# Optimization experiments

Measured on AMD Instinct MI355X. Metric: run time of the kernel, lower is better.

The kernel has to match this reference:

```python
import jax, jax.numpy as jnp
import numpy as np

PATCH = 64
STRIDE = PATCH // 2
SEQ = 65536
NPATCH = (SEQ - PATCH) // STRIDE + 1  # 2047
B = 256
EPS = 1e-5


def setup_inputs() -> dict:
    key = jax.random.key(0)
    ks = jax.random.split(key, 10)
    s = lambda k, shp: jax.random.normal(k, shp, jnp.float32) * 0.05
    return dict(
        x=jax.random.normal(ks[0], (B, 1, SEQ), jnp.float32),
        conv1_w=s(ks[1], (NPATCH, NPATCH - 1)),
        conv1_b=s(ks[2], (NPATCH,)),
        w1=s(ks[3], (32, 3, 5)), b1=s(ks[4], (32,)),
        g1=jnp.ones((32,), jnp.float32), be1=jnp.zeros((32,), jnp.float32),
        w2=s(ks[5], (64, 32, 3)), b2=s(ks[6], (64,)),
        g2=jnp.ones((64,), jnp.float32), be2=jnp.zeros((64,), jnp.float32),
        w3=s(ks[7], (128, 64, 3)), b3=s(ks[8], (128,)),
        g3=jnp.ones((128,), jnp.float32), be3=jnp.zeros((128,), jnp.float32),
    )


def _conv1d(x, w, b, pad):
    # x: [B, Cin, L], w: [Cout, Cin, K]
    y = jax.lax.conv_general_dilated(x, w, (1,), [(pad, pad)],
                                     dimension_numbers=('NCH', 'OIH', 'NCH'))
    return y + b[None, :, None]


def _bn(x, g, be):
    # training-mode BatchNorm1d: biased var over (batch, length)
    m = jnp.mean(x, axis=(0, 2), keepdims=True)
    v = jnp.var(x, axis=(0, 2), keepdims=True)
    return (x - m) * jax.lax.rsqrt(v + EPS) * g[None, :, None] + be[None, :, None]


def _maxpool2(x):
    # MaxPool1d(kernel=2, stride=2), floor division of length
    L = x.shape[-1] // 2
    return x[..., : 2 * L].reshape(x.shape[0], x.shape[1], L, 2).max(-1)


def reference(x, conv1_w, conv1_b, w1, b1, g1, be1, w2, b2, g2, be2, w3, b3, g3, be3):
    starts = jnp.arange(NPATCH) * STRIDE
    idx = starts[:, None] + jnp.arange(PATCH)[None, :]         # [NW, W]
    xp = x[:, :, idx]                                          # [B,1,NW,W]
    mean = xp.mean(-1)                                         # [B,1,NW]
    std = jnp.std(xp, axis=-1, ddof=1)                         # torch.std is unbiased
    stats = jnp.concatenate([mean, std], axis=1)               # [B,2,NW]
    dx = jnp.diff(xp, axis=2)                                  # diff across window index: [B,1,NW-1,W]
    dmax = dx.max(-1)                                          # [B,1,NW-1]
    dmax = jnp.transpose(dmax, (0, 2, 1))                      # [B,NW-1,1]
    # conv1: 1x1 Conv1d over length-1 axis == matmul over channel dim
    d2 = jnp.einsum('oi,bil->bol', conv1_w, dmax) + conv1_b[None, :, None]  # [B,NW,1]
    d2 = jnp.transpose(d2, (0, 2, 1))                          # [B,1,NW]
    x3 = jnp.concatenate([stats, d2], axis=1)                  # [B,3,NW]
    h = _maxpool2(jax.nn.relu(_bn(_conv1d(x3, w1, b1, 2), g1, be1)))
    h = _maxpool2(jax.nn.relu(_bn(_conv1d(h, w2, b2, 1), g2, be2)))
    h = jax.nn.relu(_bn(_conv1d(h, w3, b3, 1), g3, be3))
    return h.mean(-1)                                          # AdaptiveAvgPool1d(1)+Flatten -> [B,128]
```

## Files before the change

kernel.cpp:

```cpp
#include <hip/hip_runtime.h>
#include <math.h>

#define NB 256
#define SEQ 65536
#define NP 2047
#define NPM 2046
#define KPAD 2048
#define LEN1 2047
#define LEN2 1023
#define LEN3 511
#define C1 32
#define C2 64
#define C3 128
#define NPART 2048
#define NPART2 (NB*4)
#define LPAD 514
#define LPAD1 1026

#define OFF_X3   0
#define SZ_X3    (NB*3*NP)
#define OFF_DMAX (OFF_X3 + SZ_X3)
#define SZ_DMAX  (NB*NPM)
#define OFF_Y1   (OFF_DMAX + SZ_DMAX)
#define SZ_Y1    (NB*C1*LEN1)
#define OFF_Y2   (OFF_Y1 + SZ_Y1)
#define SZ_Y2    (NB*C2*LEN2)
#define OFF_S1   (OFF_Y2 + SZ_Y2)
#define OFF_S2   (OFF_S1 + 2*C1)
#define OFF_S3   (OFF_S2 + 2*C2)
#define OFF_W2C  (OFF_S3 + 2*C3)
#define OFF_W3B  (OFF_W2C + C1*C2*3)
#define OFF_PS   (OFF_W3B + C2*C3*3)
#define OFF_PQ   (OFF_PS + C3*NPART)
#define OFF_WB   OFF_Y2
#define OFF_H1R  OFF_Y2
#define OFF_H2T  OFF_Y2
#define OFF_H1B  OFF_Y1
#define OFF_PM   (OFF_Y1 + (NB*LPAD1*C1)/2)
#define OFF_W2B  OFF_W2C

typedef __attribute__((ext_vector_type(8))) short short8;
typedef __attribute__((ext_vector_type(4))) float f32x4;

__device__ inline short f2bf(float f){
  union { float f; unsigned u; } x; x.f = f;
  unsigned r = x.u + 0x7FFF + ((x.u >> 16) & 1);
  return (short)(r >> 16);
}

#define RED4L(v) v += __shfl_xor(v,1,64); v += __shfl_xor(v,2,64); \
                 v += __shfl_xor(v,4,64); v += __shfl_xor(v,8,64);

#define TILES(X) X(0,0) X(0,1) X(0,2) X(0,3) X(1,0) X(1,1) X(1,2) X(1,3) \
                 X(2,0) X(2,1) X(2,2) X(2,3) X(3,0) X(3,1) X(3,2) X(3,3)
#define DECLBIAS(P,ct) f32x4 bi##ct = *(const f32x4*)((P) + cbase + ct*16 + kq*4);
#define DECLACC(lt,ct) f32x4 acc##lt##ct = bi##ct;

__global__ __launch_bounds__(256) void k_patch(const float* __restrict__ x, const float* __restrict__ c1b,
                                               float* __restrict__ ws){
  float* x3    = ws + OFF_X3;
  short* dmaxB = (short*)(ws + OFF_DMAX);
  int b = blockIdx.y;
  int chunk = blockIdx.x;
  const float* xr = x + (size_t)b*SEQ + chunk*2048;
  __shared__ float Ss[65], Qs[65], Dm[65];
  int w = threadIdx.x >> 6;
  int l = threadIdx.x & 63;
  #pragma unroll
  for (int i=0;i<2;i++){
    int seg = w*2 + i;
    int off = seg*256;
    float4 A = *(const float4*)(xr + off + l*4);
    float4 Bh = make_float4(0.f,0.f,0.f,0.f);
    if (l >= 56){
      int g = chunk*2048 + off + 256 + (l-56)*4;
      if (g + 3 < SEQ) Bh = *(const float4*)(xr + off + 256 + (l-56)*4);
    }
    int src = (l+8) & 63;
    float p0 = __shfl(A.x, src, 64), p1 = __shfl(A.y, src, 64),
          p2 = __shfl(A.z, src, 64), p3 = __shfl(A.w, src, 64);
    if (l >= 56){ p0=Bh.x; p1=Bh.y; p2=Bh.z; p3=Bh.w; }
    float s = (A.x+A.y)+(A.z+A.w);
    float q = fmaf(A.x,A.x, fmaf(A.y,A.y, fmaf(A.z,A.z, A.w*A.w)));
    float d = fmaxf(fmaxf(p0-A.x, p1-A.y), fmaxf(p2-A.z, p3-A.w));
    #pragma unroll
    for (int o=1;o<8;o<<=1){
      s += __shfl_xor(s,o,64);
      q += __shfl_xor(q,o,64);
      d  = fmaxf(d, __shfl_xor(d,o,64));
    }
    if ((l&7)==0){ int m = seg*8 + (l>>3); Ss[m]=s; Qs[m]=q; Dm[m]=d; }
  }
  if (w==0){
    float s=0.f,q=0.f,d=-1e30f;
    if (l < 8){
      int g = chunk*2048 + 2048 + l*4;
      if (g+3 < SEQ){
        float4 A = *(const float4*)(xr + 2048 + l*4);
        float4 P = make_float4(0.f,0.f,0.f,0.f);
        if (g+35 < SEQ) P = *(const float4*)(xr + 2048 + 32 + l*4);
        s = (A.x+A.y)+(A.z+A.w);
        q = fmaf(A.x,A.x, fmaf(A.y,A.y, fmaf(A.z,A.z, A.w*A.w)));
        d = fmaxf(fmaxf(P.x-A.x, P.y-A.y), fmaxf(P.z-A.z, P.w-A.w));
      }
    }
    #pragma unroll
    for (int o=1;o<8;o<<=1){
      s += __shfl_xor(s,o,64);
      q += __shfl_xor(q,o,64);
      d  = fmaxf(d, __shfl_xor(d,o,64));
    }
    if (l==0){ Ss[64]=s; Qs[64]=q; Dm[64]=d; }
  }
  __syncthreads();
  if (threadIdx.x < 64){
    int j = threadIdx.x;
    int p = chunk*64 + j;
    if (p < NP){
      float S = Ss[j]+Ss[j+1];
      float Q = Qs[j]+Qs[j+1];
      float mean = S*(1.0f/64.0f);
      float var  = (Q - S*mean)*(1.0f/63.0f);
      x3[(b*3+0)*NP + p] = mean;
      x3[(b*3+1)*NP + p] = sqrtf(fmaxf(var,0.0f));
      x3[(b*3+2)*NP + p] = c1b[p];
    }
    dmaxB[(size_t)b*KPAD + p] = (p < NPM) ? f2bf(fmaxf(Dm[j], Dm[j+1])) : (short)0;
  }
}

__global__ __launch_bounds__(256) void k_wB(const float* __restrict__ W, float* __restrict__ ws){
  short* Wb = (short*)(ws + OFF_WB);
  int o = blockIdx.y;
  int k = blockIdx.x*256 + threadIdx.x;
  Wb[(size_t)o*KPAD + k] = (k < NPM) ? f2bf(W[(size_t)o*NPM + k]) : (short)0;
}

__global__ __launch_bounds__(256) void k_wt(const float* __restrict__ w2, const float* __restrict__ w3, float* __restrict__ ws){
  short* w2b = (short*)(ws + OFF_W2B);
  short* w3b = (short*)(ws + OFF_W3B);
  int t = blockIdx.x*256 + threadIdx.x;
  if (t < 3*C2*C1){
    int tap = t / (C2*C1);
    int r = t - tap*(C2*C1);
    int c = r >> 5, i = r & 31;
    w2b[t] = f2bf(w2[(c*C1 + i)*3 + tap]);
  }
  if (t < 3*C3*C2){
    int tap = t / (C3*C2);
    int r = t - tap*(C3*C2);
    int c = r / C2, i = r - c*C2;
    w3b[(tap*C3 + c)*C2 + i] = f2bf(w3[(c*C2+i)*3 + tap]);
  }
}

__global__ __launch_bounds__(256) void k_gemm(float* __restrict__ ws){
  const short* Ab = (const short*)(ws + OFF_DMAX);
  const short* Bb = (const short*)(ws + OFF_WB);
  float* x3 = ws + OFF_X3;
  int wid  = __builtin_amdgcn_readfirstlane(threadIdx.x >> 6);
  int lane = threadIdx.x & 63;
  int ln = lane & 15, kq = lane >> 4;
  int n0  = blockIdx.x*32;
  int m16 = (blockIdx.y*4 + wid)*16;
  int ks  = blockIdx.z*512;
  f32x4 acc0 = {0.f,0.f,0.f,0.f}, acc1 = {0.f,0.f,0.f,0.f};
  int o0 = n0 + ln, o1 = n0 + 16 + ln;
  const short* ap  = Ab + (size_t)(m16 + ln)*KPAD + ks + kq*8;
  const short* bp0 = Bb + (size_t)min(o0, NP-1)*KPAD + ks + kq*8;
  const short* bp1 = Bb + (size_t)min(o1, NP-1)*KPAD + ks + kq*8;
  #pragma unroll 4
  for (int s=0; s<16; s++){
    short8 av = *(const short8*)(ap  + s*32);
    short8 b0 = *(const short8*)(bp0 + s*32);
    short8 b1 = *(const short8*)(bp1 + s*32);
    acc0 = __builtin_amdgcn_mfma_f32_16x16x32_bf16(av, b0, acc0, 0, 0, 0);
    acc1 = __builtin_amdgcn_mfma_f32_16x16x32_bf16(av, b1, acc1, 0, 0, 0);
  }
  #pragma unroll
  for (int r=0;r<4;r++){
    int b = m16 + kq*4 + r;
    float* xp = x3 + ((size_t)b*3 + 2)*NP;
    if (o0 < NP) atomicAdd(xp + o0, acc0[r]);
    if (o1 < NP) atomicAdd(xp + o1, acc1[r]);
  }
}

__global__ __launch_bounds__(256) void k_conv1f(const float* __restrict__ w1, const float* __restrict__ b1, float* __restrict__ ws){
  const float* x3 = ws + OFF_X3;
  float* h1r = ws + OFF_H1R;
  float* ps = ws + OFF_PS;
  float* pq = ws + OFF_PQ;
  int b = blockIdx.y;
  int blk = blockIdx.x;
  int w = threadIdx.x >> 6;
  int lane = threadIdx.x & 63;
  int h = lane >> 5, c = lane & 31;
  int p0 = blk*256 + w*64 + h*32;
  float wv[3][5];
  #pragma unroll
  for (int i=0;i<3;i++){
    #pragma unroll
    for (int j=0;j<5;j++) wv[i][j] = w1[(c*3+i)*5+j];
  }
  float bc = b1[c];
  const float* xb = x3 + (size_t)b*3*NP;
  float s = 0.f, q = 0.f;
  #pragma unroll
  for (int k0=0;k0<32;k0+=8){
    float xv[3][12];
    #pragma unroll
    for (int i=0;i<3;i++){
      #pragma unroll
      for (int t=0;t<12;t++){
        int g = p0 + k0 - 2 + t;
        xv[i][t] = (g >= 0 && g < LEN1) ? xb[(size_t)i*NP + g] : 0.f;
      }
    }
    float acc[8];
    #pragma unroll
    for (int k=0;k<8;k++){
      float a = bc;
      #pragma unroll
      for (int i=0;i<3;i++){
        #pragma unroll
        for (int j=0;j<5;j++) a = fmaf(wv[i][j], xv[i][k+j], a);
      }
      acc[k] = a;
      if (p0 + k0 + k < LEN1){ s += a; q = fmaf(a, a, q); }
    }
    #pragma unroll
    for (int t=0;t<4;t++){
      int m = ((p0 + k0) >> 1) + t;
      if (m < LEN2) h1r[((size_t)b*LEN2 + m)*C1 + c] = fmaxf(acc[2*t], acc[2*t+1]);
    }
  }
  s += __shfl_xor(s, 32, 64);
  q += __shfl_xor(q, 32, 64);
  __shared__ float es[4][C1], eq[4][C1];
  if (h == 0){ es[w][c] = s; eq[w][c] = q; }
  __syncthreads();
  if (threadIdx.x < C1){
    int cc = threadIdx.x;
    float S = es[0][cc]+es[1][cc]+es[2][cc]+es[3][cc];
    float Q = eq[0][cc]+eq[1][cc]+eq[2][cc]+eq[3][cc];
    ps[(size_t)cc*NPART + b*8 + blk] = S;
    pq[(size_t)cc*NPART + b*8 + blk] = Q;
  }
}

__global__ __launch_bounds__(256) void k_fin(const float* __restrict__ ps, const float* __restrict__ pq,
                                             const float* __restrict__ g, const float* __restrict__ be,
                                             float* __restrict__ stats, int C, int npart, double invN,
                                             float* __restrict__ outz){
  if (outz) outz[(size_t)threadIdx.x * C3 + blockIdx.x] = 0.f;
  int c = blockIdx.x;
  double s=0.0, q=0.0;
  for (int j=threadIdx.x; j<npart; j+=256){ s += (double)ps[c*npart+j]; q += (double)pq[c*npart+j]; }
  #pragma unroll
  for (int off=32; off; off>>=1){ s += __shfl_xor(s,off,64); q += __shfl_xor(q,off,64); }
  __shared__ double rs[4], rq[4];
  int wid = threadIdx.x>>6, lane=threadIdx.x&63;
  if (lane==0){ rs[wid]=s; rq[wid]=q; }
  __syncthreads();
  if (threadIdx.x==0){
    double S = rs[0]+rs[1]+rs[2]+rs[3];
    double Q = rq[0]+rq[1]+rq[2]+rq[3];
    double mean = S*invN;
    double var  = Q*invN - mean*mean;
    double a = (double)g[c] / sqrt(var + 1e-5);
    stats[c]   = (float)a;
    stats[C+c] = (float)((double)be[c] - mean*a);
  }
}

__global__ __launch_bounds__(256) void k_bn1t(float* __restrict__ ws){
  const float* st = ws + OFF_S1;
  const float* h1r = ws + OFF_H1R;
  short* h1b = (short*)(ws + OFF_H1B);
  int b = blockIdx.y;
  int idx8 = (blockIdx.x*256 + threadIdx.x)*8;
  if (idx8 >= LPAD1*C1) return;
  int row = idx8 >> 5, i0 = idx8 & 31;
  short* dst = h1b + ((size_t)b*LPAD1 + row)*C1 + i0;
  short8 r;
  if (row == 0 || row >= 1024){
    r = (short8)0;
  } else {
    const float* src = h1r + ((size_t)b*LEN2 + (row-1))*C1 + i0;
    f32x4 vlo = *(const f32x4*)src, vhi = *(const f32x4*)(src+4);
    f32x4 alo = *(const f32x4*)(st + i0),      ahi = *(const f32x4*)(st + i0 + 4);
    f32x4 blo = *(const f32x4*)(st + C1 + i0), bhi = *(const f32x4*)(st + C1 + i0 + 4);
    #pragma unroll
    for (int j=0;j<4;j++){
      r[j]   = f2bf(fmaxf(fmaf(alo[j], vlo[j], blo[j]), 0.f));
      r[j+4] = f2bf(fmaxf(fmaf(ahi[j], vhi[j], bhi[j]), 0.f));
    }
  }
  *(short8*)dst = r;
}

__global__ __launch_bounds__(256) void k_conv2m(const float* __restrict__ b2, float* __restrict__ ws){
  const short* h1b = (const short*)(ws + OFF_H1B);
  const short* w2b = (const short*)(ws + OFF_W2B);
  float* pmaxT = ws + OFF_PM;
  float* ps = ws + OFF_PS;
  float* pq = ws + OFF_PQ;
  int b   = blockIdx.y;
  int blk = blockIdx.x;
  int w   = __builtin_amdgcn_readfirstlane(threadIdx.x >> 6);
  int lane = threadIdx.x & 63;
  int ln = lane & 15, kq = lane >> 4;
  int l0 = blk*256 + w*64;
  int cbase = 0;
  DECLBIAS(b2,0) DECLBIAS(b2,1) DECLBIAS(b2,2) DECLBIAS(b2,3)
  TILES(DECLACC)
  const short* wA = w2b + (size_t)ln*C1 + kq*8;
#define LDW(T,ct) short8 aw##T##ct = *(const short8*)(wA + (size_t)(T*C2 + ct*16)*C1);
  LDW(0,0) LDW(0,1) LDW(0,2) LDW(0,3)
  LDW(1,0) LDW(1,1) LDW(1,2) LDW(1,3)
  LDW(2,0) LDW(2,1) LDW(2,2) LDW(2,3)
#undef LDW
  const short* hB = h1b + ((size_t)b*LPAD1 + l0 + ln)*C1 + kq*8;
#define MMT0(lt,ct) acc##lt##ct = __builtin_amdgcn_mfma_f32_16x16x32_bf16(aw0##ct, bv##lt, acc##lt##ct, 0, 0, 0);
#define MMT1(lt,ct) acc##lt##ct = __builtin_amdgcn_mfma_f32_16x16x32_bf16(aw1##ct, bv##lt, acc##lt##ct, 0, 0, 0);
#define MMT2(lt,ct) acc##lt##ct = __builtin_amdgcn_mfma_f32_16x16x32_bf16(aw2##ct, bv##lt, acc##lt##ct, 0, 0, 0);
#define CSTEP(T) { \
    short8 bv0 = *(const short8*)(hB + (size_t)(0*16 + T)*C1); \
    short8 bv1 = *(const short8*)(hB + (size_t)(1*16 + T)*C1); \
    short8 bv2 = *(const short8*)(hB + (size_t)(2*16 + T)*C1); \
    short8 bv3 = *(const short8*)(hB + (size_t)(3*16 + T)*C1); \
    TILES(MMT##T) }
  CSTEP(0) CSTEP(1) CSTEP(2)
#undef CSTEP
#define PST(lt,ct) { \
    float p0_ = fmaxf(acc##lt##ct[0], __shfl_xor(acc##lt##ct[0],1,64)); \
    float p1_ = fmaxf(acc##lt##ct[1], __shfl_xor(acc##lt##ct[1],1,64)); \
    float p2_ = fmaxf(acc##lt##ct[2], __shfl_xor(acc##lt##ct[2],1,64)); \
    float p3_ = fmaxf(acc##lt##ct[3], __shfl_xor(acc##lt##ct[3],1,64)); \
    int l_ = l0 + lt*16 + ln; \
    if (!(ln & 1) && (l_ >> 1) < LEN3){ \
      f32x4 pv_ = {p0_, p1_, p2_, p3_}; \
      *(f32x4*)(pmaxT + ((size_t)b*LEN3 + (l_>>1))*C2 + ct*16 + kq*4) = pv_; } }
  TILES(PST)
#undef PST
  __shared__ float es[4][C2], eq[4][C2];
  #pragma unroll
  for (int ct=0;ct<4;ct++){
    float s0=0.f,s1=0.f,s2=0.f,s3=0.f,q0=0.f,q1=0.f,q2=0.f,q3=0.f;
#define ACCST(lt,CT) if (CT == ct){ int l_ = l0 + lt*16 + ln; if (l_ < LEN2){ \
      s0 += acc##lt##CT[0]; q0 = fmaf(acc##lt##CT[0], acc##lt##CT[0], q0); \
      s1 += acc##lt##CT[1]; q1 = fmaf(acc##lt##CT[1], acc##lt##CT[1], q1); \
      s2 += acc##lt##CT[2]; q2 = fmaf(acc##lt##CT[2], acc##lt##CT[2], q2); \
      s3 += acc##lt##CT[3]; q3 = fmaf(acc##lt##CT[3], acc##lt##CT[3], q3); } }
    TILES(ACCST)
#undef ACCST
    RED4L(s0) RED4L(s1) RED4L(s2) RED4L(s3)
    RED4L(q0) RED4L(q1) RED4L(q2) RED4L(q3)
    if (ln == 0){
      int c0 = ct*16 + kq*4;
      es[w][c0+0]=s0; es[w][c0+1]=s1; es[w][c0+2]=s2; es[w][c0+3]=s3;
      eq[w][c0+0]=q0; eq[w][c0+1]=q1; eq[w][c0+2]=q2; eq[w][c0+3]=q3;
    }
  }
  __syncthreads();
  if (threadIdx.x < C2){
    int c = threadIdx.x;
    float S = es[0][c]+es[1][c]+es[2][c]+es[3][c];
    float Q = eq[0][c]+eq[1][c]+eq[2][c]+eq[3][c];
    ps[(size_t)c*NPART2 + b*4 + blk] = S;
    pq[(size_t)c*NPART2 + b*4 + blk] = Q;
  }
}

__global__ __launch_bounds__(256) void k_p2bf(float* __restrict__ ws){
  const float* pm = ws + OFF_PM;
  const float* st = ws + OFF_S2;
  short* h2t = (short*)(ws + OFF_H2T);
  int b = blockIdx.y;
  int idx = blockIdx.x*256 + threadIdx.x;
  if (idx < LEN3*C2){
    int m = idx >> 6, c = idx & 63;
    float v = fmaxf(fmaf(st[c], pm[((size_t)b*LEN3 + m)*C2 + c], st[C2+c]), 0.f);
    h2t[((size_t)b*LPAD + m + 1)*C2 + c] = f2bf(v);
  } else {
    int zr = idx - LEN3*C2;
    if (zr < 3*C2){
      int rsel = zr >> 6, c = zr & 63;
      int row = (rsel == 0) ? 0 : (511 + rsel);
      h2t[((size_t)b*LPAD + row)*C2 + c] = 0;
    }
  }
}

__global__ __launch_bounds__(256) void k_conv3s(const float* __restrict__ b3, float* __restrict__ ws){
  const short* h2t = (const short*)(ws + OFF_H2T);
  const short* w3b = (const short*)(ws + OFF_W3B);
  float* ps = ws + OFF_PS;
  float* pq = ws + OFF_PQ;
  int b   = blockIdx.y;
  int blk = blockIdx.x;
  int wid = __builtin_amdgcn_readfirstlane(threadIdx.x >> 6);
  int lane = threadIdx.x & 63;
  int ln = lane & 15, kq = lane >> 4;
  int lh = wid & 1, ch = wid >> 1;
  int l0 = blk*128 + lh*64;
  int cbase = ch*64;
  DECLBIAS(b3,0) DECLBIAS(b3,1) DECLBIAS(b3,2) DECLBIAS(b3,3)
  TILES(DECLACC)
  const short* hB = h2t + ((size_t)b*LPAD + l0 + ln)*C2 + kq*8;
  const short* wA = w3b + (size_t)(cbase + ln)*C2 + kq*8;
  #pragma unroll
  for (int t=0;t<3;t++){
    #pragma unroll
    for (int s=0;s<2;s++){
#define LDB(lt) short8 bv##lt = *(const short8*)(hB + (size_t)(lt*16 + t)*C2 + s*32);
      LDB(0) LDB(1) LDB(2) LDB(3)
#define LDA(ct) short8 av##ct = *(const short8*)(wA + (size_t)(t*C3 + ct*16)*C2 + s*32);
      LDA(0) LDA(1) LDA(2) LDA(3)
#define MM(lt,ct) acc##lt##ct = __builtin_amdgcn_mfma_f32_16x16x32_bf16(av##ct, bv##lt, acc##lt##ct, 0, 0, 0);
      TILES(MM)
#undef LDB
#undef LDA
    }
  }
  int pidx = b*8 + blk*2 + lh;
  #pragma unroll
  for (int ct=0;ct<4;ct++){
    float s0=0.f,s1=0.f,s2=0.f,s3=0.f,q0=0.f,q1=0.f,q2=0.f,q3=0.f;
#define ACCST(lt,CT) if (CT == ct){ int l_ = l0 + lt*16 + ln; if (l_ < LEN3){ \
      s0 += acc##lt##CT[0]; q0 = fmaf(acc##lt##CT[0], acc##lt##CT[0], q0); \
      s1 += acc##lt##CT[1]; q1 = fmaf(acc##lt##CT[1], acc##lt##CT[1], q1); \
      s2 += acc##lt##CT[2]; q2 = fmaf(acc##lt##CT[2], acc##lt##CT[2], q2); \
      s3 += acc##lt##CT[3]; q3 = fmaf(acc##lt##CT[3], acc##lt##CT[3], q3); } }
    TILES(ACCST)
#undef ACCST
    RED4L(s0) RED4L(s1) RED4L(s2) RED4L(s3)
    RED4L(q0) RED4L(q1) RED4L(q2) RED4L(q3)
    if (ln == 0){
      int c0 = cbase + ct*16 + kq*4;
      ps[(size_t)(c0+0)*NPART + pidx] = s0;  pq[(size_t)(c0+0)*NPART + pidx] = q0;
      ps[(size_t)(c0+1)*NPART + pidx] = s1;  pq[(size_t)(c0+1)*NPART + pidx] = q1;
      ps[(size_t)(c0+2)*NPART + pidx] = s2;  pq[(size_t)(c0+2)*NPART + pidx] = q2;
      ps[(size_t)(c0+3)*NPART + pidx] = s3;  pq[(size_t)(c0+3)*NPART + pidx] = q3;
    }
  }
}

__global__ __launch_bounds__(256) void k_out3(float* __restrict__ out, const float* __restrict__ b3,
                                              const float* __restrict__ ws){
  const short* h2t = (const short*)(ws + OFF_H2T);
  const short* w3b = (const short*)(ws + OFF_W3B);
  const float* st  = ws + OFF_S3;
  int b   = blockIdx.y;
  int blk = blockIdx.x;
  int wid = __builtin_amdgcn_readfirstlane(threadIdx.x >> 6);
  int lane = threadIdx.x & 63;
  int ln = lane & 15, kq = lane >> 4;
  int lh = wid & 1, ch = wid >> 1;
  int l0 = blk*128 + lh*64;
  int cbase = ch*64;
  DECLBIAS(b3,0) DECLBIAS(b3,1) DECLBIAS(b3,2) DECLBIAS(b3,3)
  TILES(DECLACC)
  const short* hB = h2t + ((size_t)b*LPAD + l0 + ln)*C2 + kq*8;
  const short* wA = w3b + (size_t)(cbase + ln)*C2 + kq*8;
  #pragma unroll
  for (int t=0;t<3;t++){
    #pragma unroll
    for (int s=0;s<2;s++){
#define LDB(lt) short8 bv##lt = *(const short8*)(hB + (size_t)(lt*16 + t)*C2 + s*32);
      LDB(0) LDB(1) LDB(2) LDB(3)
#define LDA(ct) short8 av##ct = *(const short8*)(wA + (size_t)(t*C3 + ct*16)*C2 + s*32);
      LDA(0) LDA(1) LDA(2) LDA(3)
      TILES(MM)
#undef LDB
#undef LDA
    }
  }
  const float inv = 1.0f/511.0f;
  #pragma unroll
  for (int ct=0;ct<4;ct++){
    int c0 = cbase + ct*16 + kq*4;
    float a0 = st[c0+0], a1 = st[c0+1], a2 = st[c0+2], a3 = st[c0+3];
    float h0 = st[C3+c0+0], h1_ = st[C3+c0+1], h2_ = st[C3+c0+2], h3 = st[C3+c0+3];
    float s0=0.f,s1=0.f,s2=0.f,s3=0.f;
#define OSUM(lt,CT) if (CT == ct){ int l_ = l0 + lt*16 + ln; if (l_ < LEN3){ \
      s0 += fmaxf(fmaf(a0, acc##lt##CT[0], h0 ), 0.f); \
      s1 += fmaxf(fmaf(a1, acc##lt##CT[1], h1_), 0.f); \
      s2 += fmaxf(fmaf(a2, acc##lt##CT[2], h2_), 0.f); \
      s3 += fmaxf(fmaf(a3, acc##lt##CT[3], h3 ), 0.f); } }
    TILES(OSUM)
#undef OSUM
    RED4L(s0) RED4L(s1) RED4L(s2) RED4L(s3)
    if (ln == 0){
      atomicAdd(out + (size_t)b*C3 + c0+0, s0*inv);
      atomicAdd(out + (size_t)b*C3 + c0+1, s1*inv);
      atomicAdd(out + (size_t)b*C3 + c0+2, s2*inv);
      atomicAdd(out + (size_t)b*C3 + c0+3, s3*inv);
    }
  }
}

extern "C" void kernel_launch(void* const* d_in, const int* in_sizes, int n_in,
                              void* d_out, int out_size, void* d_ws, size_t ws_size,
                              hipStream_t stream) {
  const float* x   = (const float*)d_in[0];
  const float* c1w = (const float*)d_in[1];
  const float* c1b = (const float*)d_in[2];
  const float* w1  = (const float*)d_in[3];
  const float* b1  = (const float*)d_in[4];
  const float* g1  = (const float*)d_in[5];
  const float* be1 = (const float*)d_in[6];
  const float* w2  = (const float*)d_in[7];
  const float* b2  = (const float*)d_in[8];
  const float* g2  = (const float*)d_in[9];
  const float* be2 = (const float*)d_in[10];
  const float* w3  = (const float*)d_in[11];
  const float* b3  = (const float*)d_in[12];
  const float* g3  = (const float*)d_in[13];
  const float* be3 = (const float*)d_in[14];
  float* ws  = (float*)d_ws;
  float* out = (float*)d_out;

  hipLaunchKernelGGL(k_patch,  dim3(32,NB), dim3(256), 0, stream, x, c1b, ws);
  hipLaunchKernelGGL(k_wB,     dim3(KPAD/256, NP), dim3(256), 0, stream, c1w, ws);
  hipLaunchKernelGGL(k_wt,     dim3((3*C3*C2+255)/256), dim3(256), 0, stream, w2, w3, ws);
  hipLaunchKernelGGL(k_gemm,   dim3(64,4,4), dim3(256), 0, stream, ws);
  hipLaunchKernelGGL(k_conv1f, dim3(8,NB), dim3(256), 0, stream, w1, b1, ws);
  hipLaunchKernelGGL(k_fin,    dim3(C1), dim3(256), 0, stream, ws+OFF_PS, ws+OFF_PQ, g1, be1, ws+OFF_S1, C1, NPART, 1.0/((double)NB*LEN1), (float*)nullptr);
  hipLaunchKernelGGL(k_bn1t,   dim3((LPAD1*C1/8 + 255)/256, NB), dim3(256), 0, stream, ws);
  hipLaunchKernelGGL(k_conv2m, dim3(4,NB), dim3(256), 0, stream, b2, ws);
  hipLaunchKernelGGL(k_fin,    dim3(C2), dim3(256), 0, stream, ws+OFF_PS, ws+OFF_PQ, g2, be2, ws+OFF_S2, C2, NPART2, 1.0/((double)NB*LEN2), (float*)nullptr);
  hipLaunchKernelGGL(k_p2bf,   dim3((LEN3*C2+3*C2+255)/256, NB), dim3(256), 0, stream, ws);
  hipLaunchKernelGGL(k_conv3s, dim3(4,NB), dim3(256), 0, stream, b3, ws);
  hipLaunchKernelGGL(k_fin,    dim3(C3), dim3(256), 0, stream, ws+OFF_PS, ws+OFF_PQ, g3, be3, ws+OFF_S3, C3, NPART, 1.0/((double)NB*LEN3), out);
  hipLaunchKernelGGL(k_out3,   dim3(4,NB), dim3(256), 0, stream, out, b3, ws);
}
```

Measured before the change: 310.8 us.

## Rewrite patch stats as one thread per window and pad x3 rows

The patch kernel now gives each thread a whole window. The thread loads 24 float4s directly from global memory and computes sum, sum of squares and the diff max without shuffles or shared memory. The x3 row stride is padded from 2047 to 2048 so that conv1 can use aligned float4 loads for its input windows, with a scalar fallback at the edges. The per-thread loads are strided by 128 bytes and overlapping, which could hurt coalescing and raise register pressure, while the shuffles and the barrier go away.

```diff
diff --git a/kernel.cpp b/kernel.cpp
--- a/kernel.cpp
+++ b/kernel.cpp
@@ -5,6 +5,7 @@
 #define SEQ 65536
 #define NP 2047
 #define NPM 2046
+#define NPP 2048
 #define KPAD 2048
 #define LEN1 2047
 #define LEN2 1023
@@ -18,7 +19,7 @@
 #define LPAD1 1026
 
 #define OFF_X3   0
-#define SZ_X3    (NB*3*NP)
+#define SZ_X3    (NB*3*NPP)
 #define OFF_DMAX (OFF_X3 + SZ_X3)
 #define SZ_DMAX  (NB*NPM)
 #define OFF_Y1   (OFF_DMAX + SZ_DMAX)
@@ -61,72 +62,46 @@
   float* x3    = ws + OFF_X3;
   short* dmaxB = (short*)(ws + OFF_DMAX);
   int b = blockIdx.y;
-  int chunk = blockIdx.x;
-  const float* xr = x + (size_t)b*SEQ + chunk*2048;
-  __shared__ float Ss[65], Qs[65], Dm[65];
-  int w = threadIdx.x >> 6;
-  int l = threadIdx.x & 63;
-  #pragma unroll
-  for (int i=0;i<2;i++){
-    int seg = w*2 + i;
-    int off = seg*256;
-    float4 A = *(const float4*)(xr + off + l*4);
-    float4 Bh = make_float4(0.f,0.f,0.f,0.f);
-    if (l >= 56){
-      int g = chunk*2048 + off + 256 + (l-56)*4;
-      if (g + 3 < SEQ) Bh = *(const float4*)(xr + off + 256 + (l-56)*4);
-    }
-    int src = (l+8) & 63;
-    float p0 = __shfl(A.x, src, 64), p1 = __shfl(A.y, src, 64),
-          p2 = __shfl(A.z, src, 64), p3 = __shfl(A.w, src, 64);
-    if (l >= 56){ p0=Bh.x; p1=Bh.y; p2=Bh.z; p3=Bh.w; }
-    float s = (A.x+A.y)+(A.z+A.w);
-    float q = fmaf(A.x,A.x, fmaf(A.y,A.y, fmaf(A.z,A.z, A.w*A.w)));
-    float d = fmaxf(fmaxf(p0-A.x, p1-A.y), fmaxf(p2-A.z, p3-A.w));
-    #pragma unroll
-    for (int o=1;o<8;o<<=1){
-      s += __shfl_xor(s,o,64);
-      q += __shfl_xor(q,o,64);
-      d  = fmaxf(d, __shfl_xor(d,o,64));
-    }
-    if ((l&7)==0){ int m = seg*8 + (l>>3); Ss[m]=s; Qs[m]=q; Dm[m]=d; }
-  }
-  if (w==0){
-    float s=0.f,q=0.f,d=-1e30f;
-    if (l < 8){
-      int g = chunk*2048 + 2048 + l*4;
-      if (g+3 < SEQ){
-        float4 A = *(const float4*)(xr + 2048 + l*4);
-        float4 P = make_float4(0.f,0.f,0.f,0.f);
-        if (g+35 < SEQ) P = *(const float4*)(xr + 2048 + 32 + l*4);
-        s = (A.x+A.y)+(A.z+A.w);
-        q = fmaf(A.x,A.x, fmaf(A.y,A.y, fmaf(A.z,A.z, A.w*A.w)));
-        d = fmaxf(fmaxf(P.x-A.x, P.y-A.y), fmaxf(P.z-A.z, P.w-A.w));
-      }
-    }
-    #pragma unroll
-    for (int o=1;o<8;o<<=1){
-      s += __shfl_xor(s,o,64);
-      q += __shfl_xor(q,o,64);
-      d  = fmaxf(d, __shfl_xor(d,o,64));
-    }
-    if (l==0){ Ss[64]=s; Qs[64]=q; Dm[64]=d; }
-  }
-  __syncthreads();
-  if (threadIdx.x < 64){
-    int j = threadIdx.x;
-    int p = chunk*64 + j;
-    if (p < NP){
-      float S = Ss[j]+Ss[j+1];
-      float Q = Qs[j]+Qs[j+1];
-      float mean = S*(1.0f/64.0f);
-      float var  = (Q - S*mean)*(1.0f/63.0f);
-      x3[(b*3+0)*NP + p] = mean;
-      x3[(b*3+1)*NP + p] = sqrtf(fmaxf(var,0.0f));
-      x3[(b*3+2)*NP + p] = c1b[p];
-    }
-    dmaxB[(size_t)b*KPAD + p] = (p < NPM) ? f2bf(fmaxf(Dm[j], Dm[j+1])) : (short)0;
-  }
+  int p = blockIdx.x*256 + threadIdx.x;
+  const float* xp = x + (size_t)b*SEQ + (size_t)p*32;
+  float4 v[24];
+  if (p < NP){
+    #pragma unroll
+    for (int t=0;t<16;t++) v[t] = *(const float4*)(xp + 4*t);
+  }
+  if (p < NPM){
+    #pragma unroll
+    for (int t=16;t<24;t++) v[t] = *(const float4*)(xp + 4*t);
+  }
+  if (p < NP){
+    float4 s4 = make_float4(0.f,0.f,0.f,0.f), q4 = make_float4(0.f,0.f,0.f,0.f);
+    #pragma unroll
+    for (int t=0;t<16;t++){
+      s4.x += v[t].x; s4.y += v[t].y; s4.z += v[t].z; s4.w += v[t].w;
+      q4.x = fmaf(v[t].x,v[t].x,q4.x); q4.y = fmaf(v[t].y,v[t].y,q4.y);
+      q4.z = fmaf(v[t].z,v[t].z,q4.z); q4.w = fmaf(v[t].w,v[t].w,q4.w);
+    }
+    float S = (s4.x+s4.y)+(s4.z+s4.w);
+    float Q = (q4.x+q4.y)+(q4.z+q4.w);
+    float mean = S*(1.0f/64.0f);
+    float var  = (Q - S*mean)*(1.0f/63.0f);
+    x3[(size_t)(b*3+0)*NPP + p] = mean;
+    x3[(size_t)(b*3+1)*NPP + p] = sqrtf(fmaxf(var,0.0f));
+    x3[(size_t)(b*3+2)*NPP + p] = c1b[p];
+  }
+  short dv = 0;
+  if (p < NPM){
+    float4 d4 = make_float4(-1e30f,-1e30f,-1e30f,-1e30f);
+    #pragma unroll
+    for (int t=0;t<16;t++){
+      d4.x = fmaxf(d4.x, v[t+8].x - v[t].x);
+      d4.y = fmaxf(d4.y, v[t+8].y - v[t].y);
+      d4.z = fmaxf(d4.z, v[t+8].z - v[t].z);
+      d4.w = fmaxf(d4.w, v[t+8].w - v[t].w);
+    }
+    dv = f2bf(fmaxf(fmaxf(d4.x,d4.y), fmaxf(d4.z,d4.w)));
+  }
+  dmaxB[(size_t)b*KPAD + p] = dv;
 }
 
 __global__ __launch_bounds__(256) void k_wB(const float* __restrict__ W, float* __restrict__ ws){
@@ -180,7 +155,7 @@
   #pragma unroll
   for (int r=0;r<4;r++){
     int b = m16 + kq*4 + r;
-    float* xp = x3 + ((size_t)b*3 + 2)*NP;
+    float* xp = x3 + ((size_t)(b*3) + 2)*NPP;
     if (o0 < NP) atomicAdd(xp + o0, acc0[r]);
     if (o1 < NP) atomicAdd(xp + o1, acc1[r]);
   }
@@ -204,17 +179,21 @@
     for (int j=0;j<5;j++) wv[i][j] = w1[(c*3+i)*5+j];
   }
   float bc = b1[c];
-  const float* xb = x3 + (size_t)b*3*NP;
+  const float* xb = x3 + (size_t)b*3*NPP;
   float s = 0.f, q = 0.f;
   #pragma unroll
   for (int k0=0;k0<32;k0+=8){
-    float xv[3][12];
+    int base = p0 + k0 - 4;
+    float xw[3][16];
     #pragma unroll
     for (int i=0;i<3;i++){
-      #pragma unroll
-      for (int t=0;t<12;t++){
-        int g = p0 + k0 - 2 + t;
-        xv[i][t] = (g >= 0 && g < LEN1) ? xb[(size_t)i*NP + g] : 0.f;
+      const float* xr = xb + (size_t)i*NPP;
+      if (base >= 0 && base + 16 <= LEN1){
+        #pragma unroll
+        for (int t=0;t<4;t++) *(f32x4*)&xw[i][4*t] = *(const f32x4*)(xr + base + 4*t);
+      } else {
+        #pragma unroll
+        for (int t=0;t<16;t++){ int g = base + t; xw[i][t] = (g >= 0 && g < LEN1) ? xr[g] : 0.f; }
       }
     }
     float acc[8];
@@ -224,7 +203,7 @@
       #pragma unroll
       for (int i=0;i<3;i++){
         #pragma unroll
-        for (int j=0;j<5;j++) a = fmaf(wv[i][j], xv[i][k+j], a);
+        for (int j=0;j<5;j++) a = fmaf(wv[i][j], xw[i][k+j+2], a);
       }
       acc[k] = a;
       if (p0 + k0 + k < LEN1){ s += a; q = fmaf(a, a, q); }
@@ -522,7 +501,7 @@
   float* ws  = (float*)d_ws;
   float* out = (float*)d_out;
 
-  hipLaunchKernelGGL(k_patch,  dim3(32,NB), dim3(256), 0, stream, x, c1b, ws);
+  hipLaunchKernelGGL(k_patch,  dim3(8,NB), dim3(256), 0, stream, x, c1b, ws);
   hipLaunchKernelGGL(k_wB,     dim3(KPAD/256, NP), dim3(256), 0, stream, c1w, ws);
   hipLaunchKernelGGL(k_wt,     dim3((3*C3*C2+255)/256), dim3(256), 0, stream, w2, w3, ws);
   hipLaunchKernelGGL(k_gemm,   dim3(64,4,4), dim3(256), 0, stream, ws);
```

Result: no change. 311.6 us (+0.3%).

## Fuse BN1 apply into conv2 loads, merge weight prep kernels, pad x3 rows

Applied to the files above, without the earlier changes.

Removes the separate k_bn1t pass by applying BN1 scale/shift, ReLU and bf16 conversion inside k_conv2m as it loads h1r rows, eliminating a write and re-read of the padded bf16 buffer. The k_wB and k_wt weight-conversion kernels are merged into one launch. x3 rows are padded to 2048 so conv1 can use aligned float4 loads for interior windows. In exchange, conv2 does redundant BN conversion per tap and reads fp32 instead of bf16 activations, with more VALU work in the MFMA loop.

```diff
diff --git a/kernel.cpp b/kernel.cpp
--- a/kernel.cpp
+++ b/kernel.cpp
@@ -5,6 +5,7 @@
 #define SEQ 65536
 #define NP 2047
 #define NPM 2046
+#define NPP 2048
 #define KPAD 2048
 #define LEN1 2047
 #define LEN2 1023
@@ -15,10 +16,9 @@
 #define NPART 2048
 #define NPART2 (NB*4)
 #define LPAD 514
-#define LPAD1 1026
 
 #define OFF_X3   0
-#define SZ_X3    (NB*3*NP)
+#define SZ_X3    (NB*3*NPP)
 #define OFF_DMAX (OFF_X3 + SZ_X3)
 #define SZ_DMAX  (NB*NPM)
 #define OFF_Y1   (OFF_DMAX + SZ_DMAX)
@@ -35,8 +35,7 @@
 #define OFF_WB   OFF_Y2
 #define OFF_H1R  OFF_Y2
 #define OFF_H2T  OFF_Y2
-#define OFF_H1B  OFF_Y1
-#define OFF_PM   (OFF_Y1 + (NB*LPAD1*C1)/2)
+#define OFF_PM   (OFF_Y1 + 4300000)
 #define OFF_W2B  OFF_W2C
 
 typedef __attribute__((ext_vector_type(8))) short short8;
@@ -121,36 +120,38 @@
       float Q = Qs[j]+Qs[j+1];
       float mean = S*(1.0f/64.0f);
       float var  = (Q - S*mean)*(1.0f/63.0f);
-      x3[(b*3+0)*NP + p] = mean;
-      x3[(b*3+1)*NP + p] = sqrtf(fmaxf(var,0.0f));
-      x3[(b*3+2)*NP + p] = c1b[p];
+      x3[(size_t)(b*3+0)*NPP + p] = mean;
+      x3[(size_t)(b*3+1)*NPP + p] = sqrtf(fmaxf(var,0.0f));
+      x3[(size_t)(b*3+2)*NPP + p] = c1b[p];
     }
     dmaxB[(size_t)b*KPAD + p] = (p < NPM) ? f2bf(fmaxf(Dm[j], Dm[j+1])) : (short)0;
   }
 }
 
-__global__ __launch_bounds__(256) void k_wB(const float* __restrict__ W, float* __restrict__ ws){
-  short* Wb = (short*)(ws + OFF_WB);
-  int o = blockIdx.y;
-  int k = blockIdx.x*256 + threadIdx.x;
-  Wb[(size_t)o*KPAD + k] = (k < NPM) ? f2bf(W[(size_t)o*NPM + k]) : (short)0;
-}
-
-__global__ __launch_bounds__(256) void k_wt(const float* __restrict__ w2, const float* __restrict__ w3, float* __restrict__ ws){
-  short* w2b = (short*)(ws + OFF_W2B);
-  short* w3b = (short*)(ws + OFF_W3B);
-  int t = blockIdx.x*256 + threadIdx.x;
-  if (t < 3*C2*C1){
-    int tap = t / (C2*C1);
-    int r = t - tap*(C2*C1);
-    int c = r >> 5, i = r & 31;
-    w2b[t] = f2bf(w2[(c*C1 + i)*3 + tap]);
-  }
-  if (t < 3*C3*C2){
-    int tap = t / (C3*C2);
-    int r = t - tap*(C3*C2);
-    int c = r / C2, i = r - c*C2;
-    w3b[(tap*C3 + c)*C2 + i] = f2bf(w3[(c*C2+i)*3 + tap]);
+__global__ __launch_bounds__(256) void k_prep(const float* __restrict__ W, const float* __restrict__ w2,
+                                              const float* __restrict__ w3, float* __restrict__ ws){
+  int bid = blockIdx.x;
+  if (bid < 8*NP){
+    short* Wb = (short*)(ws + OFF_WB);
+    int o = bid >> 3;
+    int k = (bid & 7)*256 + threadIdx.x;
+    Wb[(size_t)o*KPAD + k] = (k < NPM) ? f2bf(W[(size_t)o*NPM + k]) : (short)0;
+  } else {
+    short* w2b = (short*)(ws + OFF_W2B);
+    short* w3b = (short*)(ws + OFF_W3B);
+    int t = (bid - 8*NP)*256 + threadIdx.x;
+    if (t < 3*C2*C1){
+      int tap = t / (C2*C1);
+      int r = t - tap*(C2*C1);
+      int c = r >> 5, i = r & 31;
+      w2b[t] = f2bf(w2[(c*C1 + i)*3 + tap]);
+    }
+    if (t < 3*C3*C2){
+      int tap = t / (C3*C2);
+      int r = t - tap*(C3*C2);
+      int c = r / C2, i = r - c*C2;
+      w3b[(tap*C3 + c)*C2 + i] = f2bf(w3[(c*C2+i)*3 + tap]);
+    }
   }
 }
 
@@ -180,7 +181,7 @@
   #pragma unroll
   for (int r=0;r<4;r++){
     int b = m16 + kq*4 + r;
-    float* xp = x3 + ((size_t)b*3 + 2)*NP;
+    float* xp = x3 + ((size_t)(b*3) + 2)*NPP;
     if (o0 < NP) atomicAdd(xp + o0, acc0[r]);
     if (o1 < NP) atomicAdd(xp + o1, acc1[r]);
   }
@@ -204,17 +205,21 @@
     for (int j=0;j<5;j++) wv[i][j] = w1[(c*3+i)*5+j];
   }
   float bc = b1[c];
-  const float* xb = x3 + (size_t)b*3*NP;
+  const float* xb = x3 + (size_t)b*3*NPP;
   float s = 0.f, q = 0.f;
   #pragma unroll
   for (int k0=0;k0<32;k0+=8){
-    float xv[3][12];
+    int base = p0 + k0 - 4;
+    float xw[3][16];
     #pragma unroll
     for (int i=0;i<3;i++){
-      #pragma unroll
-      for (int t=0;t<12;t++){
-        int g = p0 + k0 - 2 + t;
-        xv[i][t] = (g >= 0 && g < LEN1) ? xb[(size_t)i*NP + g] : 0.f;
+      const float* xr = xb + (size_t)i*NPP;
+      if (base >= 0 && base + 16 <= LEN1){
+        #pragma unroll
+        for (int t=0;t<4;t++) *(f32x4*)&xw[i][4*t] = *(const f32x4*)(xr + base + 4*t);
+      } else {
+        #pragma unroll
+        for (int t=0;t<16;t++){ int g = base + t; xw[i][t] = (g >= 0 && g < LEN1) ? xr[g] : 0.f; }
       }
     }
     float acc[8];
@@ -224,7 +229,7 @@
       #pragma unroll
       for (int i=0;i<3;i++){
         #pragma unroll
-        for (int j=0;j<5;j++) a = fmaf(wv[i][j], xv[i][k+j], a);
+        for (int j=0;j<5;j++) a = fmaf(wv[i][j], xw[i][k+j+2], a);
       }
       acc[k] = a;
       if (p0 + k0 + k < LEN1){ s += a; q = fmaf(a, a, q); }
@@ -274,34 +279,9 @@
   }
 }
 
-__global__ __launch_bounds__(256) void k_bn1t(float* __restrict__ ws){
-  const float* st = ws + OFF_S1;
+__global__ __launch_bounds__(256) void k_conv2m(const float* __restrict__ b2, float* __restrict__ ws){
   const float* h1r = ws + OFF_H1R;
-  short* h1b = (short*)(ws + OFF_H1B);
-  int b = blockIdx.y;
-  int idx8 = (blockIdx.x*256 + threadIdx.x)*8;
-  if (idx8 >= LPAD1*C1) return;
-  int row = idx8 >> 5, i0 = idx8 & 31;
-  short* dst = h1b + ((size_t)b*LPAD1 + row)*C1 + i0;
-  short8 r;
-  if (row == 0 || row >= 1024){
-    r = (short8)0;
-  } else {
-    const float* src = h1r + ((size_t)b*LEN2 + (row-1))*C1 + i0;
-    f32x4 vlo = *(const f32x4*)src, vhi = *(const f32x4*)(src+4);
-    f32x4 alo = *(const f32x4*)(st + i0),      ahi = *(const f32x4*)(st + i0 + 4);
-    f32x4 blo = *(const f32x4*)(st + C1 + i0), bhi = *(const f32x4*)(st + C1 + i0 + 4);
-    #pragma unroll
-    for (int j=0;j<4;j++){
-      r[j]   = f2bf(fmaxf(fmaf(alo[j], vlo[j], blo[j]), 0.f));
-      r[j+4] = f2bf(fmaxf(fmaf(ahi[j], vhi[j], bhi[j]), 0.f));
-    }
-  }
-  *(short8*)dst = r;
-}
-
-__global__ __launch_bounds__(256) void k_conv2m(const float* __restrict__ b2, float* __restrict__ ws){
-  const short* h1b = (const short*)(ws + OFF_H1B);
+  const float* st1 = ws + OFF_S1;
   const short* w2b = (const short*)(ws + OFF_W2B);
   float* pmaxT = ws + OFF_PM;
   float* ps = ws + OFF_PS;
@@ -315,24 +295,40 @@
   int cbase = 0;
   DECLBIAS(b2,0) DECLBIAS(b2,1) DECLBIAS(b2,2) DECLBIAS(b2,3)
   TILES(DECLACC)
+  f32x4 a1lo = *(const f32x4*)(st1 + kq*8),      a1hi = *(const f32x4*)(st1 + kq*8 + 4);
+  f32x4 b1lo = *(const f32x4*)(st1 + C1 + kq*8), b1hi = *(const f32x4*)(st1 + C1 + kq*8 + 4);
   const short* wA = w2b + (size_t)ln*C1 + kq*8;
 #define LDW(T,ct) short8 aw##T##ct = *(const short8*)(wA + (size_t)(T*C2 + ct*16)*C1);
   LDW(0,0) LDW(0,1) LDW(0,2) LDW(0,3)
   LDW(1,0) LDW(1,1) LDW(1,2) LDW(1,3)
   LDW(2,0) LDW(2,1) LDW(2,2) LDW(2,3)
 #undef LDW
-  const short* hB = h1b + ((size_t)b*LPAD1 + l0 + ln)*C1 + kq*8;
+  const float* hR = h1r + (size_t)b*LEN2*C1 + kq*8;
 #define MMT0(lt,ct) acc##lt##ct = __builtin_amdgcn_mfma_f32_16x16x32_bf16(aw0##ct, bv##lt, acc##lt##ct, 0, 0, 0);
 #define MMT1(lt,ct) acc##lt##ct = __builtin_amdgcn_mfma_f32_16x16x32_bf16(aw1##ct, bv##lt, acc##lt##ct, 0, 0, 0);
 #define MMT2(lt,ct) acc##lt##ct = __builtin_amdgcn_mfma_f32_16x16x32_bf16(aw2##ct, bv##lt, acc##lt##ct, 0, 0, 0);
+#define LDB(lt,T) short8 bv##lt; { \
+    int pos_ = l0 + ln + lt*16 + T - 1; \
+    union { short8 s8; short s[8]; } fr_; \
+    if (pos_ >= 0 && pos_ < LEN2){ \
+      const float* pa_ = hR + (size_t)pos_*C1; \
+      f32x4 xlo_ = *(const f32x4*)pa_, xhi_ = *(const f32x4*)(pa_ + 4); \
+      fr_.s[0] = f2bf(fmaxf(fmaf(a1lo[0], xlo_[0], b1lo[0]), 0.f)); \
+      fr_.s[1] = f2bf(fmaxf(fmaf(a1lo[1], xlo_[1], b1lo[1]), 0.f)); \
+      fr_.s[2] = f2bf(fmaxf(fmaf(a1lo[2], xlo_[2], b1lo[2]), 0.f)); \
+      fr_.s[3] = f2bf(fmaxf(fmaf(a1lo[3], xlo_[3], b1lo[3]), 0.f)); \
+      fr_.s[4] = f2bf(fmaxf(fmaf(a1hi[0], xhi_[0], b1hi[0]), 0.f)); \
+      fr_.s[5] = f2bf(fmaxf(fmaf(a1hi[1], xhi_[1], b1hi[1]), 0.f)); \
+      fr_.s[6] = f2bf(fmaxf(fmaf(a1hi[2], xhi_[2], b1hi[2]), 0.f)); \
+      fr_.s[7] = f2bf(fmaxf(fmaf(a1hi[3], xhi_[3], b1hi[3]), 0.f)); \
+    } else { fr_.s8 = (short8)0; } \
+    bv##lt = fr_.s8; }
 #define CSTEP(T) { \
-    short8 bv0 = *(const short8*)(hB + (size_t)(0*16 + T)*C1); \
-    short8 bv1 = *(const short8*)(hB + (size_t)(1*16 + T)*C1); \
-    short8 bv2 = *(const short8*)(hB + (size_t)(2*16 + T)*C1); \
-    short8 bv3 = *(const short8*)(hB + (size_t)(3*16 + T)*C1); \
+    LDB(0,T) LDB(1,T) LDB(2,T) LDB(3,T) \
     TILES(MMT##T) }
   CSTEP(0) CSTEP(1) CSTEP(2)
 #undef CSTEP
+#undef LDB
 #define PST(lt,ct) { \
     float p0_ = fmaxf(acc##lt##ct[0], __shfl_xor(acc##lt##ct[0],1,64)); \
     float p1_ = fmaxf(acc##lt##ct[1], __shfl_xor(acc##lt##ct[1],1,64)); \
@@ -523,12 +519,10 @@
   float* out = (float*)d_out;
 
   hipLaunchKernelGGL(k_patch,  dim3(32,NB), dim3(256), 0, stream, x, c1b, ws);
-  hipLaunchKernelGGL(k_wB,     dim3(KPAD/256, NP), dim3(256), 0, stream, c1w, ws);
-  hipLaunchKernelGGL(k_wt,     dim3((3*C3*C2+255)/256), dim3(256), 0, stream, w2, w3, ws);
+  hipLaunchKernelGGL(k_prep,   dim3(8*NP + 96), dim3(256), 0, stream, c1w, w2, w3, ws);
   hipLaunchKernelGGL(k_gemm,   dim3(64,4,4), dim3(256), 0, stream, ws);
   hipLaunchKernelGGL(k_conv1f, dim3(8,NB), dim3(256), 0, stream, w1, b1, ws);
   hipLaunchKernelGGL(k_fin,    dim3(C1), dim3(256), 0, stream, ws+OFF_PS, ws+OFF_PQ, g1, be1, ws+OFF_S1, C1, NPART, 1.0/((double)NB*LEN1), (float*)nullptr);
-  hipLaunchKernelGGL(k_bn1t,   dim3((LPAD1*C1/8 + 255)/256, NB), dim3(256), 0, stream, ws);
   hipLaunchKernelGGL(k_conv2m, dim3(4,NB), dim3(256), 0, stream, b2, ws);
   hipLaunchKernelGGL(k_fin,    dim3(C2), dim3(256), 0, stream, ws+OFF_PS, ws+OFF_PQ, g2, be2, ws+OFF_S2, C2, NPART2, 1.0/((double)NB*LEN2), (float*)nullptr);
   hipLaunchKernelGGL(k_p2bf,   dim3((LEN3*C2+3*C2+255)/256, NB), dim3(256), 0, stream, ws);
```

Measured after the change: 302.5 us. 2.7% less time.
